# Performance work log

Hardware: AMD Instinct MI355X
Metric: run time of the kernel (lower is better)

Reference implementation:

```python
import jax, jax.numpy as jnp
import numpy as np

B, N, F_IN = 512, 128, 133
NHID, NHEADS, HID = 64, 8, 512
FP_DIM, FP2, TASKS = 1489, 512, 12
ALPHA = 0.2
NEG_BIG = -9e15


def _lin_init(key, fan_in, fan_out):
    return jax.random.normal(key, (fan_in, fan_out), jnp.float32) / np.sqrt(fan_in)


def setup_inputs() -> dict:
    key = jax.random.key(0)
    ks = jax.random.split(key, 24)
    inp = {
        'h': jax.random.normal(ks[0], (B, N, F_IN), jnp.float32),
        'adj': jax.random.randint(ks[1], (B, N, N), 0, 2, jnp.int32),
        'edge_feat': jax.random.uniform(ks[2], (B, N, N), jnp.float32),
        'fp': jax.random.uniform(ks[3], (B, FP_DIM), jnp.float32),
        # multi-head GAT layer params (a split as [a1; a2; a_edge])
        'W_heads': jax.random.normal(ks[4], (NHEADS, F_IN, NHID), jnp.float32) / np.sqrt(F_IN),
        'a1_heads': jax.random.normal(ks[5], (NHEADS, NHID), jnp.float32) / np.sqrt(NHID),
        'a2_heads': jax.random.normal(ks[6], (NHEADS, NHID), jnp.float32) / np.sqrt(NHID),
        'ae_heads': jax.random.normal(ks[7], (NHEADS,), jnp.float32) * 0.1,
        # output GAT layer
        'W_out': jax.random.normal(ks[8], (NHID * NHEADS, HID), jnp.float32) / np.sqrt(NHID * NHEADS),
        'a1_out': jax.random.normal(ks[9], (HID,), jnp.float32) / np.sqrt(HID),
        'a2_out': jax.random.normal(ks[10], (HID,), jnp.float32) / np.sqrt(HID),
        'ae_out': jax.random.normal(ks[11], ()) * 0.1,
        # FPN
        'fc1_w': _lin_init(ks[12], FP_DIM, FP2), 'fc1_b': jnp.zeros((FP2,), jnp.float32),
        'fc2_w': _lin_init(ks[13], FP2, HID), 'fc2_b': jnp.zeros((HID,), jnp.float32),
        # cross-attention fusion
        'q_w': _lin_init(ks[14], HID, HID), 'q_b': jnp.zeros((HID,), jnp.float32),
        'k_w': _lin_init(ks[15], HID, HID), 'k_b': jnp.zeros((HID,), jnp.float32),
        'v_w': _lin_init(ks[16], HID, HID), 'v_b': jnp.zeros((HID,), jnp.float32),
        'o_w': _lin_init(ks[17], HID, HID), 'o_b': jnp.zeros((HID,), jnp.float32),
        # FFN head
        'ffn1_w': _lin_init(ks[18], HID, HID), 'ffn1_b': jnp.zeros((HID,), jnp.float32),
        'ffn2_w': _lin_init(ks[19], HID, TASKS), 'ffn2_b': jnp.zeros((TASKS,), jnp.float32),
    }
    return inp


def _leaky(x):
    return jnp.where(x >= 0, x, ALPHA * x)


def _fpgnn_forward(h, adj, edge_feat, fp,
                   W_heads, a1_heads, a2_heads, ae_heads,
                   W_out, a1_out, a2_out, ae_out,
                   fc1_w, fc1_b, fc2_w, fc2_b,
                   q_w, q_b, k_w, k_b, v_w, v_b, o_w, o_b,
                   ffn1_w, ffn1_b, ffn2_w, ffn2_b):
    mask = adj > 0  # [B,N,N]
    # --- multi-head GAT layers (concat=True) ---
    Wh = jnp.einsum('bnf,hfd->bhnd', h, W_heads)            # [B,H,N,D]
    s1 = jnp.einsum('bhnd,hd->bhn', Wh, a1_heads)
    s2 = jnp.einsum('bhnd,hd->bhn', Wh, a2_heads)
    # e[b,h,i,j] = leaky(Wh_i.a1 + Wh_j.a2 + edge_ij*ae)  (exact decomposition of
    # the original concat([Wh_i, Wh_j, edge_ij]) @ a)
    e = _leaky(s1[:, :, :, None] + s2[:, :, None, :]
               + edge_feat[:, None, :, :] * ae_heads[None, :, None, None])
    att = jnp.where(mask[:, None], e, NEG_BIG)
    att = jax.nn.softmax(att, axis=-1)                       # softmax over dim=1 of [N,N]
    hp = jnp.einsum('bhij,bhjd->bhid', att, Wh)
    x = jax.nn.elu(hp)                                       # concat=True -> ELU
    x = jnp.transpose(x, (0, 2, 1, 3)).reshape(B, N, NHEADS * NHID)
    # --- output GAT layer (concat=False) ---
    Wx = x @ W_out                                           # [B,N,HID]
    t1 = Wx @ a1_out                                         # [B,N]
    t2 = Wx @ a2_out
    e2 = _leaky(t1[:, :, None] + t2[:, None, :] + edge_feat * ae_out)
    att2 = jnp.where(mask, e2, NEG_BIG)
    att2 = jax.nn.softmax(att2, axis=-1)
    hp2 = jnp.einsum('bij,bjd->bid', att2, Wx)
    gat_nodes = jax.nn.elu(hp2)                              # F.elu in GATOne
    gat_out = gat_nodes.mean(axis=1)                         # molecule readout [B,HID]
    # --- FPN ---
    fpn_out = jax.nn.relu(fp @ fc1_w + fc1_b) @ fc2_w + fc2_b  # [B,HID]
    # --- cross-attention fusion ---
    q = gat_out @ q_w + q_b
    k = fpn_out @ k_w + k_b
    v = fpn_out @ v_w + v_b
    score = jnp.sum(q * k, axis=-1, keepdims=True) / np.sqrt(HID)  # [B,1]
    weight = jax.nn.softmax(score[:, :, None], axis=-1)[:, :, 0]    # softmax over size-1 dim -> ones
    fused = q + weight * v
    fused = jax.nn.relu(fused @ o_w + o_b)
    # --- FFN head (dropout p=0, eval) ---
    out = jax.nn.relu(fused @ ffn1_w + ffn1_b) @ ffn2_w + ffn2_b
    return out


def reference(h, adj, edge_feat, fp,
              W_heads, a1_heads, a2_heads, ae_heads,
              W_out, a1_out, a2_out, ae_out,
              fc1_w, fc1_b, fc2_w, fc2_b,
              q_w, q_b, k_w, k_b, v_w, v_b, o_w, o_b,
              ffn1_w, ffn1_b, ffn2_w, ffn2_b):
    return _fpgnn_forward(h, adj, edge_feat, fp,
                          W_heads, a1_heads, a2_heads, ae_heads,
                          W_out, a1_out, a2_out, ae_out,
                          fc1_w, fc1_b, fc2_w, fc2_b,
                          q_w, q_b, k_w, k_b, v_w, v_b, o_w, o_b,
                          ffn1_w, ffn1_b, ffn2_w, ffn2_b)
```

## Files before the change

kernel.cpp:

```cpp
#include <hip/hip_runtime.h>
#include <hip/hip_bf16.h>


#define ALPHA_LK 0.2f
#define LOG2E 1.44269504f
#define KP1 192
#define KPF 1536
#define MINF_BF16 0xFF80u

typedef unsigned short ushort_t;
typedef __attribute__((ext_vector_type(8))) short bfrag;
typedef __attribute__((ext_vector_type(4))) float ffrag;

__device__ __forceinline__ float b2f(ushort_t u) {
  return __uint_as_float(((unsigned)u) << 16);
}
__device__ __forceinline__ ushort_t f2b(float f) {
  unsigned u = __float_as_uint(f);
  unsigned r = (u + 0x7fffu + ((u >> 16) & 1u)) >> 16;
  return (ushort_t)r;
}
__device__ __forceinline__ unsigned cvt_pk(float lo, float hi) {
  unsigned r;
  asm("v_cvt_pk_bf16_f32 %0, %1, %2" : "=v"(r) : "v"(lo), "v"(hi));
  return r;
}
__device__ __forceinline__ float frcp(float x) {
  float r;
  asm("v_rcp_f32 %0, %1" : "=v"(r) : "v"(x));
  return r;
}
__device__ __forceinline__ float fexp2(float x) {
#if __has_builtin(__builtin_amdgcn_exp2f)
  return __builtin_amdgcn_exp2f(x);
#else
  return exp2f(x);
#endif
}
__device__ __forceinline__ float elu1(float v) {
  return v > 0.f ? v : __expf(v) - 1.f;
}

__device__ __forceinline__ void gll16(const void* g, void* l) {
  __builtin_amdgcn_global_load_lds(
      (const __attribute__((address_space(1))) unsigned int*)(unsigned long long)g,
      (__attribute__((address_space(3))) unsigned int*)(unsigned long long)l,
      16, 0, 0);
}

__global__ __launch_bounds__(256) void prep_all(
    const float* __restrict__ h, const int* __restrict__ adj,
    const float* __restrict__ edge, const float* __restrict__ fp,
    const float* __restrict__ Whd, const float* __restrict__ a1h,
    const float* __restrict__ a2h,
    const float* __restrict__ W_out, const float* __restrict__ a1o,
    const float* __restrict__ a2o,
    const float* __restrict__ fc1_w, const float* __restrict__ fc2_w,
    const float* __restrict__ q_w, const float* __restrict__ v_w,
    const float* __restrict__ o_w, const float* __restrict__ ffn1_w,
    const float* __restrict__ qb, const float* __restrict__ vb,
    ushort_t* __restrict__ hb, ushort_t* __restrict__ em,
    ushort_t* __restrict__ W2t, ushort_t* __restrict__ fpb,
    ushort_t* __restrict__ fc1t,
    ushort_t* __restrict__ Wot, ushort_t* __restrict__ fc2t,
    ushort_t* __restrict__ qwt, ushort_t* __restrict__ vwt,
    ushort_t* __restrict__ owt, ushort_t* __restrict__ f1t,
    float* __restrict__ wa1, float* __restrict__ wa2,
    ushort_t* __restrict__ wh12, float* __restrict__ qvb) {
  int bid = blockIdx.x;
  const int t = threadIdx.x;

  if (bid < 8) {
    int hh = bid;
    if (t < 192) {
      float s1 = 0.f, s2 = 0.f;
      if (t < 133) {
        const float* wr = Whd + (size_t)(hh * 133 + t) * 64;
        const float* a1r = a1h + hh * 64;
        const float* a2r = a2h + hh * 64;
#pragma unroll 8
        for (int d = 0; d < 64; ++d) {
          float wv = wr[d];
          s1 += wv * a1r[d];
          s2 += wv * a2r[d];
        }
      }
      wh12[hh * 384 + t] = f2b(s1);
      wh12[hh * 384 + 192 + t] = f2b(s2);
    }
    return;
  }
  bid -= 8;
  if (bid < 128) {
    int wv = t >> 6, lane = t & 63;
    int k = bid * 4 + wv;
    const float* wr = W_out + (size_t)k * 512;
    float p1 = 0.f, p2 = 0.f;
#pragma unroll
    for (int i = 0; i < 8; ++i) {
      float v = wr[lane + i * 64];
      p1 += v * a1o[lane + i * 64];
      p2 += v * a2o[lane + i * 64];
    }
#pragma unroll
    for (int off = 32; off; off >>= 1) {
      p1 += __shfl_down(p1, off);
      p2 += __shfl_down(p2, off);
    }
    if (lane == 0) { wa1[k] = p1; wa2[k] = p2; }
    return;
  }
  bid -= 128;
  if (bid < 2) {
    int o = bid * 256 + t;
    qvb[o] = qb[o] + vb[o];
    return;
  }
  bid -= 2;
  if (bid < 96) {
    int o = bid * 256 + t;
    if (o < 512 * 48) {
      int col = o / 48, c4 = (o - col * 48) * 4;
      int hh = col >> 6, d = col & 63;
      ushort4 v;
      v.x = (c4 + 0 < 133) ? f2b(Whd[(hh * 133 + c4 + 0) * 64 + d]) : (ushort_t)0;
      v.y = (c4 + 1 < 133) ? f2b(Whd[(hh * 133 + c4 + 1) * 64 + d]) : (ushort_t)0;
      v.z = (c4 + 2 < 133) ? f2b(Whd[(hh * 133 + c4 + 2) * 64 + d]) : (ushort_t)0;
      v.w = (c4 + 3 < 133) ? f2b(Whd[(hh * 133 + c4 + 3) * 64 + d]) : (ushort_t)0;
      *(ushort4*)&W2t[(size_t)col * KP1 + c4] = v;
    }
    return;
  }
  bid -= 96;
  if (bid < 768) {
    int o = bid * 256 + t;
    int row = o / 384, c4 = (o - row * 384) * 4;
    const float* fr = fp + (size_t)row * 1489;
    ushort4 v;
    v.x = (c4 + 0 < 1489) ? f2b(fr[c4 + 0]) : (ushort_t)0;
    v.y = (c4 + 1 < 1489) ? f2b(fr[c4 + 1]) : (ushort_t)0;
    v.z = (c4 + 2 < 1489) ? f2b(fr[c4 + 2]) : (ushort_t)0;
    v.w = (c4 + 3 < 1489) ? f2b(fr[c4 + 3]) : (ushort_t)0;
    *(ushort4*)&fpb[(size_t)row * KPF + c4] = v;
    return;
  }
  bid -= 768;
  if (bid < 768) {
    int o = bid * 256 + t;
    int col = o / 384, k4 = (o - col * 384) * 4;
    ushort4 v;
    v.x = (k4 + 0 < 1489) ? f2b(fc1_w[(size_t)(k4 + 0) * 512 + col]) : (ushort_t)0;
    v.y = (k4 + 1 < 1489) ? f2b(fc1_w[(size_t)(k4 + 1) * 512 + col]) : (ushort_t)0;
    v.z = (k4 + 2 < 1489) ? f2b(fc1_w[(size_t)(k4 + 2) * 512 + col]) : (ushort_t)0;
    v.w = (k4 + 3 < 1489) ? f2b(fc1_w[(size_t)(k4 + 3) * 512 + col]) : (ushort_t)0;
    *(ushort4*)&fc1t[(size_t)col * KPF + k4] = v;
    return;
  }
  bid -= 768;
  if (bid < 1536) {
    int y = bid >> 8;
    int o = (bid & 255) * 256 + t;
    const float* W = y == 0 ? W_out : y == 1 ? fc2_w : y == 2 ? q_w
                   : y == 3 ? v_w : y == 4 ? o_w : ffn1_w;
    ushort_t* Wt = y == 0 ? Wot : y == 1 ? fc2t : y == 2 ? qwt
                 : y == 3 ? vwt : y == 4 ? owt : f1t;
    int col = o >> 7, k4 = (o & 127) * 4;
    ushort4 v;
    v.x = f2b(W[(size_t)(k4 + 0) * 512 + col]);
    v.y = f2b(W[(size_t)(k4 + 1) * 512 + col]);
    v.z = f2b(W[(size_t)(k4 + 2) * 512 + col]);
    v.w = f2b(W[(size_t)(k4 + 3) * 512 + col]);
    *(ushort4*)&Wt[(size_t)col * 512 + k4] = v;
    return;
  }
  bid -= 1536;
  if (bid < 12288) {
    int o = bid * 256 + t;
    int row = o / 48, c4 = (o - row * 48) * 4;
    const float* hr = h + (size_t)row * 133;
    ushort4 v;
    v.x = (c4 + 0 < 133) ? f2b(hr[c4 + 0]) : (ushort_t)0;
    v.y = (c4 + 1 < 133) ? f2b(hr[c4 + 1]) : (ushort_t)0;
    v.z = (c4 + 2 < 133) ? f2b(hr[c4 + 2]) : (ushort_t)0;
    v.w = (c4 + 3 < 133) ? f2b(hr[c4 + 3]) : (ushort_t)0;
    *(ushort4*)&hb[(size_t)row * KP1 + c4] = v;
    return;
  }
  bid -= 12288;
  {
    size_t o = ((size_t)bid * 256 + t) * 4;
    float4 e = *(const float4*)&edge[o];
    int4 a = *(const int4*)&adj[o];
    ushort4 v;
    v.x = a.x > 0 ? f2b(e.x) : (ushort_t)MINF_BF16;
    v.y = a.y > 0 ? f2b(e.y) : (ushort_t)MINF_BF16;
    v.z = a.z > 0 ? f2b(e.z) : (ushort_t)MINF_BF16;
    v.w = a.w > 0 ? f2b(e.w) : (ushort_t)MINF_BF16;
    *(ushort4*)&em[o] = v;
  }
}

__global__ __launch_bounds__(256) void att2t(
    const ushort_t* __restrict__ xb, const ushort_t* __restrict__ em,
    const float* __restrict__ wa1, const float* __restrict__ wa2,
    const float* __restrict__ aeo,
    ushort_t* __restrict__ awg, float* __restrict__ sinvg, int base) {
  __shared__ float t1s[128], t2s[128];
  __shared__ float was1[512], was2[512];
  const int bl = blockIdx.x, bg = base + bl;
  const int t = threadIdx.x;
  was1[t] = wa1[t]; was1[t + 256] = wa1[t + 256];
  was2[t] = wa2[t]; was2[t + 256] = wa2[t + 256];
  __syncthreads();
  const int row = t >> 1, half = t & 1;
  {
    const ushort_t* xr = xb + (size_t)(bl * 128 + row) * 512 + half * 256;
    float p1 = 0.f, p2 = 0.f;
#pragma unroll 4
    for (int i = 0; i < 32; ++i) {
      uint4 u = *(const uint4*)&xr[i * 8];
      const unsigned uu[4] = {u.x, u.y, u.z, u.w};
#pragma unroll
      for (int pr = 0; pr < 4; ++pr) {
        float lo = __uint_as_float(uu[pr] << 16);
        float hi = __uint_as_float(uu[pr] & 0xffff0000u);
        int c = half * 256 + i * 8 + pr * 2;
        p1 = fmaf(lo, was1[c], p1); p1 = fmaf(hi, was1[c + 1], p1);
        p2 = fmaf(lo, was2[c], p2); p2 = fmaf(hi, was2[c + 1], p2);
      }
    }
    p1 += __shfl_xor(p1, 1);
    p2 += __shfl_xor(p2, 1);
    if (!half) { t1s[row] = p1 * LOG2E; t2s[row] = p2 * LOG2E; }
  }
  __syncthreads();
  const float ae2 = aeo[0] * LOG2E;
  const float rt1 = t1s[row];
  const ushort_t* emr = em + (size_t)bg * 16384 + row * 128 + half * 64;
  ushort_t* awr = awg + (size_t)bl * 16384 + row * 128 + half * 64;
  float s = 0.f;
#pragma unroll
  for (int v = 0; v < 8; ++v) {
    uint4 eu = *(const uint4*)&emr[v * 8];
    const unsigned uu[4] = {eu.x, eu.y, eu.z, eu.w};
    unsigned po[4];
#pragma unroll
    for (int pr = 0; pr < 4; ++pr) {
      float elo = __uint_as_float(uu[pr] << 16);
      float ehi = __uint_as_float(uu[pr] & 0xffff0000u);
      float e0 = fmaf(elo, ae2, rt1 + t2s[half * 64 + v * 8 + pr * 2]);
      float e1 = fmaf(ehi, ae2, rt1 + t2s[half * 64 + v * 8 + pr * 2 + 1]);
      e0 = fmaxf(e0, ALPHA_LK * e0);
      e1 = fmaxf(e1, ALPHA_LK * e1);
      float p0 = (elo != -INFINITY) ? fexp2(e0) : 0.f;
      float p1 = (ehi != -INFINITY) ? fexp2(e1) : 0.f;
      unsigned q = cvt_pk(p0, p1);
      po[pr] = q;
      s += __uint_as_float(q << 16) + __uint_as_float(q & 0xffff0000u);
    }
    *(uint4*)&awr[v * 8] = make_uint4(po[0], po[1], po[2], po[3]);
  }
  s += __shfl_xor(s, 1);
  if (!half) sinvg[(size_t)bl * 128 + row] = 1.f / fmaxf(s, 1e-30f);
}

__global__ __launch_bounds__(256) void fused_gat1(
    const ushort_t* __restrict__ hb, const ushort_t* __restrict__ W2t,
    const ushort_t* __restrict__ edgeM, const ushort_t* __restrict__ wh12g,
    const float* __restrict__ ae,
    ushort_t* __restrict__ x, int base) {
  __shared__ union {
    struct { ushort_t As[128][64]; ushort_t Bs[64][64]; } g;
    ushort_t WS[64][136];
  } u;
  __shared__ float ss1[128], ss2[128];
  __shared__ ushort_t wh12s[2][192];
  const int id = blockIdx.x;
  const int hh = (id >> 3) & 7;
  const int bl = ((id >> 6) << 3) | (id & 7);
  const int bg = base + bl;
  const int t = threadIdx.x;
  const int lane = t & 63, w = t >> 6;
  const int l16 = lane & 15, quad = lane >> 4;
  const int w8 = w * 8, sr8 = (t >> 3) & 7;
  const int csw = ((t & 7) ^ sr8) << 3;

  if (t < 96)
    *(ushort4*)&(&wh12s[0][0])[t * 4] =
        *(const ushort4*)&wh12g[hh * 384 + t * 4];

  const ushort_t* gA = hb + (size_t)(bl * 128 + w8 + sr8) * KP1 + csw;
  const ushort_t* gB = W2t + (size_t)(hh * 64 + w8 + sr8) * KP1 + csw;
  ffrag acc[2][4];
  ffrag acc_s[2];
#pragma unroll
  for (int mi = 0; mi < 2; ++mi) {
    acc_s[mi] = {0.f, 0.f, 0.f, 0.f};
#pragma unroll
    for (int ni = 0; ni < 4; ++ni) acc[mi][ni] = {0.f, 0.f, 0.f, 0.f};
  }
  for (int k0 = 0; k0 < KP1; k0 += 64) {
    __syncthreads();
#pragma unroll
    for (int p = 0; p < 4; ++p)
      gll16(gA + (size_t)(p * 32) * KP1 + k0, &u.g.As[p * 32 + w8][0]);
#pragma unroll
    for (int p = 0; p < 2; ++p)
      gll16(gB + (size_t)(p * 32) * KP1 + k0, &u.g.Bs[p * 32 + w8][0]);
    __syncthreads();
#pragma unroll
    for (int ks = 0; ks < 2; ++ks) {
      const int cs = ((ks * 4 + quad) ^ (l16 & 7)) << 3;
      bfrag af[2], bf[4];
      bfrag bs = {0, 0, 0, 0, 0, 0, 0, 0};
      if (l16 < 2)
        bs = *(const bfrag*)&wh12s[l16][k0 + ks * 32 + quad * 8];
#pragma unroll
      for (int mi = 0; mi < 2; ++mi)
        af[mi] = *(const bfrag*)&u.g.As[w * 32 + mi * 16 + l16][cs];
#pragma unroll
      for (int ni = 0; ni < 4; ++ni)
        bf[ni] = *(const bfrag*)&u.g.Bs[ni * 16 + l16][cs];
#pragma unroll
      for (int mi = 0; mi < 2; ++mi) {
#pragma unroll
        for (int ni = 0; ni < 4; ++ni)
          acc[mi][ni] = __builtin_amdgcn_mfma_f32_16x16x32_bf16(
              af[mi], bf[ni], acc[mi][ni], 0, 0, 0);
        acc_s[mi] = __builtin_amdgcn_mfma_f32_16x16x32_bf16(
            af[mi], bs, acc_s[mi], 0, 0, 0);
      }
    }
  }
  __syncthreads();

#pragma unroll
  for (int mi = 0; mi < 2; ++mi)
#pragma unroll
    for (int ni = 0; ni < 4; ++ni) {
      int col = ni * 16 + l16;
      int rowb = w * 32 + mi * 16 + quad * 4;
      uint2 pv;
      pv.x = cvt_pk(acc[mi][ni][0], acc[mi][ni][1]);
      pv.y = cvt_pk(acc[mi][ni][2], acc[mi][ni][3]);
      *(uint2*)&u.WS[col][rowb] = pv;
    }
  if (l16 < 2) {
    float* sp = (l16 == 0) ? ss1 : ss2;
#pragma unroll
    for (int mi = 0; mi < 2; ++mi)
#pragma unroll
      for (int r = 0; r < 4; ++r)
        sp[w * 32 + mi * 16 + quad * 4 + r] = acc_s[mi][r] * LOG2E;
  }
  uint4 ereg[2][4];
  {
    const ushort_t* em = edgeM + (size_t)bg * 16384;
#pragma unroll
    for (int mi = 0; mi < 2; ++mi) {
      int row = w * 32 + mi * 16 + l16;
#pragma unroll
      for (int ks = 0; ks < 4; ++ks)
        ereg[mi][ks] = *(const uint4*)&em[row * 128 + ks * 32 + quad * 8];
    }
  }
  __syncthreads();

  const float aeh2 = ae[hh] * LOG2E;
  float rs1[2];
  rs1[0] = ss1[w * 32 + l16];
  rs1[1] = ss1[w * 32 + 16 + l16];
  uint4 aw[2][4];
#pragma unroll
  for (int mi = 0; mi < 2; ++mi) {
#pragma unroll
    for (int ks = 0; ks < 4; ++ks) {
      float s2v[8];
      *(float4*)&s2v[0] = *(const float4*)&ss2[ks * 32 + quad * 8];
      *(float4*)&s2v[4] = *(const float4*)&ss2[ks * 32 + quad * 8 + 4];
      const unsigned uu[4] = {ereg[mi][ks].x, ereg[mi][ks].y,
                              ereg[mi][ks].z, ereg[mi][ks].w};
      unsigned po[4];
#pragma unroll
      for (int pr = 0; pr < 4; ++pr) {
        float elo = __uint_as_float(uu[pr] << 16);
        float ehi = __uint_as_float(uu[pr] & 0xffff0000u);
        float e0 = fmaf(elo, aeh2, rs1[mi] + s2v[pr * 2]);
        float e1 = fmaf(ehi, aeh2, rs1[mi] + s2v[pr * 2 + 1]);
        e0 = fmaxf(e0, ALPHA_LK * e0);
        e1 = fmaxf(e1, ALPHA_LK * e1);
        float p0 = (elo != -INFINITY) ? fexp2(e0) : 0.f;
        float p1 = (ehi != -INFINITY) ? fexp2(e1) : 0.f;
        po[pr] = cvt_pk(p0, p1);
      }
      aw[mi][ks] = make_uint4(po[0], po[1], po[2], po[3]);
    }
  }

  bfrag bones;
#pragma unroll
  for (int i = 0; i < 8; ++i) bones[i] = (short)0x3F80;

  ffrag acc2[2][4];
  ffrag accs[2];
#pragma unroll
  for (int mi = 0; mi < 2; ++mi) {
    accs[mi] = {0.f, 0.f, 0.f, 0.f};
#pragma unroll
    for (int ni = 0; ni < 4; ++ni) acc2[mi][ni] = {0.f, 0.f, 0.f, 0.f};
  }
#pragma unroll
  for (int ks = 0; ks < 4; ++ks) {
    bfrag bfr[4];
#pragma unroll
    for (int ni = 0; ni < 4; ++ni)
      bfr[ni] = *(const bfrag*)&u.WS[ni * 16 + l16][ks * 32 + quad * 8];
#pragma unroll
    for (int mi = 0; mi < 2; ++mi) {
      bfrag afr;
      __builtin_memcpy(&afr, &aw[mi][ks], 16);
#pragma unroll
      for (int ni = 0; ni < 4; ++ni)
        acc2[mi][ni] = __builtin_amdgcn_mfma_f32_16x16x32_bf16(
            afr, bfr[ni], acc2[mi][ni], 0, 0, 0);
      accs[mi] = __builtin_amdgcn_mfma_f32_16x16x32_bf16(
          afr, bones, accs[mi], 0, 0, 0);
    }
  }
  float sv[2][4];
#pragma unroll
  for (int mi = 0; mi < 2; ++mi)
#pragma unroll
    for (int r = 0; r < 4; ++r)
      sv[mi][r] = frcp(fmaxf(accs[mi][r], 1e-30f));

#pragma unroll
  for (int mi = 0; mi < 2; ++mi)
#pragma unroll
    for (int ni = 0; ni < 4; ++ni) {
      float e0 = elu1(acc2[mi][ni][0] * sv[mi][0]);
      float e1 = elu1(acc2[mi][ni][1] * sv[mi][1]);
      float e2 = elu1(acc2[mi][ni][2] * sv[mi][2]);
      float e3 = elu1(acc2[mi][ni][3] * sv[mi][3]);
      unsigned p01 = cvt_pk(e0, e1), p23 = cvt_pk(e2, e3);
      int rl = w * 32 + mi * 16 + quad * 4;
      size_t bo = (size_t)(bl * 128 + rl) * 512 + hh * 64 + ni * 16 + l16;
      x[bo] = (ushort_t)p01;
      x[bo + 512] = (ushort_t)(p01 >> 16);
      x[bo + 1024] = (ushort_t)p23;
      x[bo + 1536] = (ushort_t)(p23 >> 16);
    }
}

__global__ __launch_bounds__(256) void fused_gat2(
    const ushort_t* __restrict__ xb, const ushort_t* __restrict__ Wot,
    const ushort_t* __restrict__ awg, const float* __restrict__ sinvg,
    ushort_t* __restrict__ gatb, int base) {
  __shared__ union {
    struct { ushort_t As[128][64]; ushort_t Bs[128][64]; } g;
    ushort_t WS[128][136];
  } u;
  __shared__ float ps[4][64];
  const int id = blockIdx.x;
  const int sp2 = (id >> 3) & 3;
  const int bl = ((id >> 5) << 3) | (id & 7);
  const int bg = base + bl;
  const int t = threadIdx.x;
  const int lane = t & 63, w = t >> 6;
  const int wm = w >> 1, wn = w & 1;
  const int l16 = lane & 15, quad = lane >> 4;
  const int w8 = w * 8, sr8 = (t >> 3) & 7;
  const int csw = ((t & 7) ^ sr8) << 3;

  const ushort_t* gA = xb + (size_t)(bl * 128 + w8 + sr8) * 512 + csw;
  const ushort_t* gB = Wot + (size_t)(sp2 * 128 + w8 + sr8) * 512 + csw;
  ffrag acc[4][4];
#pragma unroll
  for (int mi = 0; mi < 4; ++mi)
#pragma unroll
    for (int ni = 0; ni < 4; ++ni) acc[mi][ni] = {0.f, 0.f, 0.f, 0.f};
  for (int k0 = 0; k0 < 512; k0 += 64) {
    __syncthreads();
#pragma unroll
    for (int p = 0; p < 4; ++p) {
      gll16(gA + (size_t)(p * 32) * 512 + k0, &u.g.As[p * 32 + w8][0]);
      gll16(gB + (size_t)(p * 32) * 512 + k0, &u.g.Bs[p * 32 + w8][0]);
    }
    __syncthreads();
#pragma unroll
    for (int ks = 0; ks < 2; ++ks) {
      const int cs = ((ks * 4 + quad) ^ (l16 & 7)) << 3;
      bfrag af[4], bf[4];
#pragma unroll
      for (int i = 0; i < 4; ++i) {
        af[i] = *(const bfrag*)&u.g.As[wm * 64 + i * 16 + l16][cs];
        bf[i] = *(const bfrag*)&u.g.Bs[wn * 64 + i * 16 + l16][cs];
      }
#pragma unroll
      for (int mi = 0; mi < 4; ++mi)
#pragma unroll
        for (int ni = 0; ni < 4; ++ni)
          acc[mi][ni] = __builtin_amdgcn_mfma_f32_16x16x32_bf16(
              af[mi], bf[ni], acc[mi][ni], 0, 0, 0);
    }
  }
  __syncthreads();

#pragma unroll
  for (int mi = 0; mi < 4; ++mi)
#pragma unroll
    for (int ni = 0; ni < 4; ++ni) {
      int col = wn * 64 + ni * 16 + l16;
      int rowb = wm * 64 + mi * 16 + quad * 4;
      uint2 pv;
      pv.x = cvt_pk(acc[mi][ni][0], acc[mi][ni][1]);
      pv.y = cvt_pk(acc[mi][ni][2], acc[mi][ni][3]);
      *(uint2*)&u.WS[col][rowb] = pv;
    }
  __syncthreads();

  uint4 awf[2][4];
  float sv[2][4];
  {
    const ushort_t* ap = awg + (size_t)bl * 16384;
#pragma unroll
    for (int mi = 0; mi < 2; ++mi) {
      int row = w * 32 + mi * 16 + l16;
#pragma unroll
      for (int ks = 0; ks < 4; ++ks)
        awf[mi][ks] = *(const uint4*)&ap[row * 128 + ks * 32 + quad * 8];
      float si = sinvg[(size_t)bl * 128 + row];
#pragma unroll
      for (int r = 0; r < 4; ++r) sv[mi][r] = __shfl(si, quad * 4 + r);
    }
  }

  for (int s0 = 0; s0 < 2; ++s0) {
    ffrag acc2[2][4];
#pragma unroll
    for (int mi = 0; mi < 2; ++mi)
#pragma unroll
      for (int ni = 0; ni < 4; ++ni) acc2[mi][ni] = {0.f, 0.f, 0.f, 0.f};
#pragma unroll
    for (int ks = 0; ks < 4; ++ks) {
      bfrag bfr[4];
#pragma unroll
      for (int ni = 0; ni < 4; ++ni)
        bfr[ni] = *(const bfrag*)&u.WS[s0 * 64 + ni * 16 + l16][ks * 32 + quad * 8];
#pragma unroll
      for (int mi = 0; mi < 2; ++mi) {
        bfrag afr;
        __builtin_memcpy(&afr, &awf[mi][ks], 16);
#pragma unroll
        for (int ni = 0; ni < 4; ++ni)
          acc2[mi][ni] = __builtin_amdgcn_mfma_f32_16x16x32_bf16(
              afr, bfr[ni], acc2[mi][ni], 0, 0, 0);
      }
    }
    __syncthreads();
#pragma unroll
    for (int ni = 0; ni < 4; ++ni) {
      float s = 0.f;
#pragma unroll
      for (int mi = 0; mi < 2; ++mi)
#pragma unroll
        for (int r = 0; r < 4; ++r) s += elu1(acc2[mi][ni][r] * sv[mi][r]);
      s += __shfl_xor(s, 16);
      s += __shfl_xor(s, 32);
      if (quad == 0) ps[w][ni * 16 + l16] = s;
    }
    __syncthreads();
    if (t < 64) {
      float s = ps[0][t] + ps[1][t] + ps[2][t] + ps[3][t];
      gatb[(size_t)bg * 512 + sp2 * 128 + s0 * 64 + t] = f2b(s * (1.f / 128.f));
    }
  }
}

__device__ __forceinline__ void tail_kloop(
    const ushort_t* __restrict__ A, const ushort_t* __restrict__ Bt,
    int K, int ld, ushort_t (*As)[64], ushort_t (*Bs)[64],
    ffrag (*acc)[4], int row0, int col0, int t) {
  const int lane = t & 63, w = t >> 6;
  const int wm = w >> 1, wn = w & 1;
  const int l16 = lane & 15, quad = lane >> 4;
  const int w8 = w * 8, sr8 = (t >> 3) & 7;
  const int csw = ((t & 7) ^ sr8) << 3;
  const ushort_t* gA = A + (size_t)(row0 + w8 + sr8) * ld + csw;
  const ushort_t* gB = Bt + (size_t)(col0 + w8 + sr8) * ld + csw;
  for (int k0 = 0; k0 < K; k0 += 64) {
    __syncthreads();
#pragma unroll
    for (int p = 0; p < 4; ++p) {
      gll16(gA + (size_t)(p * 32) * ld + k0, &As[p * 32 + w8][0]);
      gll16(gB + (size_t)(p * 32) * ld + k0, &Bs[p * 32 + w8][0]);
    }
    __syncthreads();
#pragma unroll
    for (int ks = 0; ks < 2; ++ks) {
      const int cs = ((ks * 4 + quad) ^ (l16 & 7)) << 3;
      bfrag af[4], bf[4];
#pragma unroll
      for (int i = 0; i < 4; ++i) {
        af[i] = *(const bfrag*)&As[wm * 64 + i * 16 + l16][cs];
        bf[i] = *(const bfrag*)&Bs[wn * 64 + i * 16 + l16][cs];
      }
#pragma unroll
      for (int mi = 0; mi < 4; ++mi)
#pragma unroll
        for (int ni = 0; ni < 4; ++ni)
          acc[mi][ni] = __builtin_amdgcn_mfma_f32_16x16x32_bf16(
              af[mi], bf[ni], acc[mi][ni], 0, 0, 0);
    }
  }
}

template <int DUAL, int RELU>
__global__ __launch_bounds__(256) void gemm_tail(
    const ushort_t* __restrict__ A1, const ushort_t* __restrict__ Bt1,
    int K1, int ld1,
    const ushort_t* __restrict__ A2, const ushort_t* __restrict__ Bt2,
    const float* __restrict__ bias, ushort_t* __restrict__ C) {
  __shared__ ushort_t As[128][64];
  __shared__ ushort_t Bs[128][64];
  const int t = threadIdx.x;
  const int lane = t & 63, w = t >> 6;
  const int wm = w >> 1, wn = w & 1;
  const int l16 = lane & 15, quad = lane >> 4;
  const int row0 = blockIdx.y * 128, col0 = blockIdx.x * 128;

  ffrag acc[4][4];
#pragma unroll
  for (int mi = 0; mi < 4; ++mi)
#pragma unroll
    for (int ni = 0; ni < 4; ++ni) acc[mi][ni] = {0.f, 0.f, 0.f, 0.f};

  tail_kloop(A1, Bt1, K1, ld1, As, Bs, acc, row0, col0, t);
  if (DUAL) tail_kloop(A2, Bt2, 512, 512, As, Bs, acc, row0, col0, t);

#pragma unroll
  for (int mi = 0; mi < 4; ++mi)
#pragma unroll
    for (int ni = 0; ni < 4; ++ni) {
      int col = col0 + wn * 64 + ni * 16 + l16;
      float bb = bias[col];
      float v0 = acc[mi][ni][0] + bb, v1 = acc[mi][ni][1] + bb;
      float v2 = acc[mi][ni][2] + bb, v3 = acc[mi][ni][3] + bb;
      if (RELU) {
        v0 = fmaxf(v0, 0.f); v1 = fmaxf(v1, 0.f);
        v2 = fmaxf(v2, 0.f); v3 = fmaxf(v3, 0.f);
      }
      unsigned p01 = cvt_pk(v0, v1), p23 = cvt_pk(v2, v3);
      int row = row0 + wm * 64 + mi * 16 + quad * 4;
      size_t o = (size_t)row * 512 + col;
      C[o] = (ushort_t)p01;
      C[o + 512] = (ushort_t)(p01 >> 16);
      C[o + 1024] = (ushort_t)p23;
      C[o + 1536] = (ushort_t)(p23 >> 16);
    }
}

__global__ __launch_bounds__(256) void ffn2_kernel(
    const ushort_t* __restrict__ f5, const float* __restrict__ W,
    const float* __restrict__ b, float* __restrict__ out) {
  int wv = threadIdx.x >> 6, lane = threadIdx.x & 63;
  int row = blockIdx.x * 4 + wv;
  const ushort_t* fr = f5 + (size_t)row * 512;
  float v[8];
  ushort4 u0 = *(const ushort4*)&fr[lane * 8];
  ushort4 u1 = *(const ushort4*)&fr[lane * 8 + 4];
  v[0] = b2f(u0.x); v[1] = b2f(u0.y); v[2] = b2f(u0.z); v[3] = b2f(u0.w);
  v[4] = b2f(u1.x); v[5] = b2f(u1.y); v[6] = b2f(u1.z); v[7] = b2f(u1.w);
#pragma unroll
  for (int j = 0; j < 12; ++j) {
    float s = 0.f;
#pragma unroll
    for (int i = 0; i < 8; ++i) s += v[i] * W[(size_t)(lane * 8 + i) * 12 + j];
#pragma unroll
    for (int off = 32; off; off >>= 1) s += __shfl_down(s, off);
    if (lane == 0) out[(size_t)row * 12 + j] = s + b[j];
  }
}

extern "C" void kernel_launch(void* const* d_in, const int* in_sizes, int n_in,
                              void* d_out, int out_size, void* d_ws, size_t ws_size,
                              hipStream_t stream) {
  const float* h        = (const float*)d_in[0];
  const int*   adj      = (const int*)d_in[1];
  const float* edge     = (const float*)d_in[2];
  const float* fp       = (const float*)d_in[3];
  const float* W_heads  = (const float*)d_in[4];
  const float* a1_heads = (const float*)d_in[5];
  const float* a2_heads = (const float*)d_in[6];
  const float* ae_heads = (const float*)d_in[7];
  const float* W_out  = (const float*)d_in[8];
  const float* a1_out = (const float*)d_in[9];
  const float* a2_out = (const float*)d_in[10];
  const float* ae_out = (const float*)d_in[11];
  const float* fc1_w = (const float*)d_in[12];
  const float* fc1_b = (const float*)d_in[13];
  const float* fc2_w = (const float*)d_in[14];
  const float* fc2_b = (const float*)d_in[15];
  const float* q_w = (const float*)d_in[16];
  const float* q_b = (const float*)d_in[17];
  const float* v_w = (const float*)d_in[20];
  const float* v_b = (const float*)d_in[21];
  const float* o_w = (const float*)d_in[22];
  const float* o_b = (const float*)d_in[23];
  const float* ffn1_w = (const float*)d_in[24];
  const float* ffn1_b = (const float*)d_in[25];
  const float* ffn2_w = (const float*)d_in[26];
  const float* ffn2_b = (const float*)d_in[27];
  float* out = (float*)d_out;

  const size_t hb_bytes = (size_t)65536 * KP1 * 2;
  const size_t em_bytes = (size_t)512 * 16384 * 2;
  const size_t tail_bytes =
      (size_t)512 * KPF * 2 * 2 + (size_t)512 * 512 * 2 * 12 + 2048;
  const size_t fixed_bytes = hb_bytes + em_bytes + (size_t)512 * KP1 * 2 +
                             (size_t)2 * 65536 * 4 + tail_bytes + 16384;
  int C = 32;
  for (int cand = 512; cand >= 32; cand >>= 1) {
    size_t need = (size_t)cand * (131072 + 32768 + 512) + fixed_bytes;
    if (need <= ws_size) { C = cand; break; }
  }
  const int M = C * 128;
  (void)M;

  char* p = (char*)d_ws;
  ushort_t* xb  = (ushort_t*)p; p += (size_t)C * 65536 * 2;
  ushort_t* awg = (ushort_t*)p; p += (size_t)C * 16384 * 2;
  float* sinv   = (float*)p;    p += (size_t)C * 128 * 4;
  ushort_t* hb  = (ushort_t*)p; p += hb_bytes;
  ushort_t* em  = (ushort_t*)p; p += em_bytes;
  ushort_t* W2t = (ushort_t*)p; p += (size_t)512 * KP1 * 2;
  ushort_t* wh12 = (ushort_t*)p; p += 8 * 384 * 2;
  float* t_unused = (float*)p; p += 2 * 65536 * 4 - 8 * 384 * 2;
  (void)t_unused;
  ushort_t* fpb  = (ushort_t*)p; p += (size_t)512 * KPF * 2;
  ushort_t* fc1t = (ushort_t*)p; p += (size_t)512 * KPF * 2;
  ushort_t* Wot  = (ushort_t*)p; p += (size_t)512 * 512 * 2;
  ushort_t* fc2t = (ushort_t*)p; p += (size_t)512 * 512 * 2;
  ushort_t* qwt  = (ushort_t*)p; p += (size_t)512 * 512 * 2;
  ushort_t* vwt  = (ushort_t*)p; p += (size_t)512 * 512 * 2;
  ushort_t* owt  = (ushort_t*)p; p += (size_t)512 * 512 * 2;
  ushort_t* f1t  = (ushort_t*)p; p += (size_t)512 * 512 * 2;
  ushort_t* gatb = (ushort_t*)p; p += (size_t)512 * 512 * 2;
  ushort_t* fb1  = (ushort_t*)p; p += (size_t)512 * 512 * 2;
  ushort_t* fb2  = (ushort_t*)p; p += (size_t)512 * 512 * 2;
  ushort_t* fb3  = (ushort_t*)p; p += (size_t)512 * 512 * 2;
  ushort_t* fb4  = (ushort_t*)p; p += (size_t)512 * 512 * 2;
  ushort_t* fb5  = (ushort_t*)p; p += (size_t)512 * 512 * 2;
  float* qvb = (float*)p; p += 2048;
  float* wa1 = (float*)p; p += 2048;
  float* wa2 = (float*)p; p += 2048;

  prep_all<<<23786, 256, 0, stream>>>(
      h, adj, edge, fp, W_heads, a1_heads, a2_heads,
      W_out, a1_out, a2_out,
      fc1_w, fc2_w, q_w, v_w, o_w, ffn1_w, q_b, v_b,
      hb, em, W2t, fpb, fc1t, Wot, fc2t, qwt, vwt, owt, f1t,
      wa1, wa2, wh12, qvb);

  for (int base = 0; base < 512; base += C) {
    fused_gat1<<<8 * C, 256, 0, stream>>>(
        hb + (size_t)base * 128 * KP1, W2t, em, wh12, ae_heads, xb, base);
    att2t<<<C, 256, 0, stream>>>(xb, em, wa1, wa2, ae_out, awg, sinv, base);
    fused_gat2<<<4 * C, 256, 0, stream>>>(xb, Wot, awg, sinv, gatb, base);
  }

  gemm_tail<0, 1><<<dim3(4, 4), 256, 0, stream>>>(
      fpb, fc1t, KPF, KPF, nullptr, nullptr, fc1_b, fb1);
  gemm_tail<0, 0><<<dim3(4, 4), 256, 0, stream>>>(
      fb1, fc2t, 512, 512, nullptr, nullptr, fc2_b, fb2);
  gemm_tail<1, 0><<<dim3(4, 4), 256, 0, stream>>>(
      gatb, qwt, 512, 512, fb2, vwt, qvb, fb3);
  gemm_tail<0, 1><<<dim3(4, 4), 256, 0, stream>>>(
      fb3, owt, 512, 512, nullptr, nullptr, o_b, fb4);
  gemm_tail<0, 1><<<dim3(4, 4), 256, 0, stream>>>(
      fb4, f1t, 512, 512, nullptr, nullptr, ffn1_b, fb5);
  ffn2_kernel<<<128, 256, 0, stream>>>(fb5, ffn2_w, ffn2_b, out);
}
```

Baseline: 425.6 us.

## Overlap FPN GEMMs with GAT stages and merge tail GEMMs via grid barrier

The fc1 and fc2 tail GEMMs now run as extra blocks inside the first attention and second GAT launches, so they overlap with the per-chunk graph work. The remaining q/v, o, ffn1 and ffn2 stages are merged into one 16-block kernel that uses an atomic-counter software barrier between stages, replacing five separate launches. Kernels now take a single parameter struct. The spin barrier relies on all 16 blocks being resident at once and on the counter being reset in prep. gat1 now indexes hb by the global batch index instead of receiving an offset pointer.

Result: slower. 585.0 us (+37.5%).

```diff
diff --git a/kernel.cpp b/kernel.cpp
--- a/kernel.cpp
+++ b/kernel.cpp
@@ -40,7 +40,6 @@
 __device__ __forceinline__ float elu1(float v) {
   return v > 0.f ? v : __expf(v) - 1.f;
 }
-
 __device__ __forceinline__ void gll16(const void* g, void* l) {
   __builtin_amdgcn_global_load_lds(
       (const __attribute__((address_space(1))) unsigned int*)(unsigned long long)g,
@@ -48,36 +47,56 @@
       16, 0, 0);
 }
 
-__global__ __launch_bounds__(256) void prep_all(
-    const float* __restrict__ h, const int* __restrict__ adj,
-    const float* __restrict__ edge, const float* __restrict__ fp,
-    const float* __restrict__ Whd, const float* __restrict__ a1h,
-    const float* __restrict__ a2h,
-    const float* __restrict__ W_out, const float* __restrict__ a1o,
-    const float* __restrict__ a2o,
-    const float* __restrict__ fc1_w, const float* __restrict__ fc2_w,
-    const float* __restrict__ q_w, const float* __restrict__ v_w,
-    const float* __restrict__ o_w, const float* __restrict__ ffn1_w,
-    const float* __restrict__ qb, const float* __restrict__ vb,
-    ushort_t* __restrict__ hb, ushort_t* __restrict__ em,
-    ushort_t* __restrict__ W2t, ushort_t* __restrict__ fpb,
-    ushort_t* __restrict__ fc1t,
-    ushort_t* __restrict__ Wot, ushort_t* __restrict__ fc2t,
-    ushort_t* __restrict__ qwt, ushort_t* __restrict__ vwt,
-    ushort_t* __restrict__ owt, ushort_t* __restrict__ f1t,
-    float* __restrict__ wa1, float* __restrict__ wa2,
-    ushort_t* __restrict__ wh12, float* __restrict__ qvb) {
-  int bid = blockIdx.x;
+struct MP {
+  const float *h; const int *adj; const float *edge; const float *fp;
+  const float *Whd, *a1h, *a2h, *aeh;
+  const float *W_out, *a1o, *a2o, *aeo;
+  const float *fc1_w, *fc1_b, *fc2_w, *fc2_b;
+  const float *q_b, *v_b, *q_w, *v_w, *o_w, *o_b;
+  const float *ffn1_w, *ffn1_b, *ffn2_w, *ffn2_b;
+  ushort_t *hb, *em, *W2t, *wh12, *fpb, *fc1t, *Wot, *fc2t, *qwt, *vwt, *owt, *f1t;
+  ushort_t *xb, *awg; float *sinv;
+  ushort_t *gatb, *fb1, *fb2, *fb3, *fb4, *fb5;
+  float *wa1, *wa2, *qvb; float *out;
+  unsigned *cnt;
+  int C;
+};
+
+struct LdsGat1 {
+  union { struct { ushort_t As[128][64]; ushort_t Bs[64][64]; } g;
+          ushort_t WS[64][136]; } u;
+  float ss1[128], ss2[128];
+  ushort_t wh12s[2][192];
+};
+struct LdsGat2 {
+  union { struct { ushort_t As[128][64]; ushort_t Bs[128][64]; } g;
+          ushort_t WS[128][136]; } u;
+  float ps[4][64];
+};
+struct LdsAtt { float t1s[128], t2s[128], was1[512], was2[512]; };
+struct LdsTail { ushort_t As[128][64]; ushort_t Bs[128][64]; };
+
+__device__ __forceinline__ void tbar(unsigned* cnt, unsigned target) {
+  __syncthreads();
+  __threadfence();
+  if (threadIdx.x == 0) {
+    atomicAdd(cnt, 1u);
+    while (atomicAdd(cnt, 0u) < target) __builtin_amdgcn_s_sleep(1);
+  }
+  __syncthreads();
+  __threadfence();
+}
+
+__device__ void prep_body(int bid, const MP& P) {
   const int t = threadIdx.x;
-
   if (bid < 8) {
     int hh = bid;
     if (t < 192) {
       float s1 = 0.f, s2 = 0.f;
       if (t < 133) {
-        const float* wr = Whd + (size_t)(hh * 133 + t) * 64;
-        const float* a1r = a1h + hh * 64;
-        const float* a2r = a2h + hh * 64;
+        const float* wr = P.Whd + (size_t)(hh * 133 + t) * 64;
+        const float* a1r = P.a1h + hh * 64;
+        const float* a2r = P.a2h + hh * 64;
 #pragma unroll 8
         for (int d = 0; d < 64; ++d) {
           float wv = wr[d];
@@ -85,8 +104,8 @@
           s2 += wv * a2r[d];
         }
       }
-      wh12[hh * 384 + t] = f2b(s1);
-      wh12[hh * 384 + 192 + t] = f2b(s2);
+      P.wh12[hh * 384 + t] = f2b(s1);
+      P.wh12[hh * 384 + 192 + t] = f2b(s2);
     }
     return;
   }
@@ -94,26 +113,27 @@
   if (bid < 128) {
     int wv = t >> 6, lane = t & 63;
     int k = bid * 4 + wv;
-    const float* wr = W_out + (size_t)k * 512;
+    const float* wr = P.W_out + (size_t)k * 512;
     float p1 = 0.f, p2 = 0.f;
 #pragma unroll
     for (int i = 0; i < 8; ++i) {
       float v = wr[lane + i * 64];
-      p1 += v * a1o[lane + i * 64];
-      p2 += v * a2o[lane + i * 64];
+      p1 += v * P.a1o[lane + i * 64];
+      p2 += v * P.a2o[lane + i * 64];
     }
 #pragma unroll
     for (int off = 32; off; off >>= 1) {
       p1 += __shfl_down(p1, off);
       p2 += __shfl_down(p2, off);
     }
-    if (lane == 0) { wa1[k] = p1; wa2[k] = p2; }
+    if (lane == 0) { P.wa1[k] = p1; P.wa2[k] = p2; }
     return;
   }
   bid -= 128;
   if (bid < 2) {
     int o = bid * 256 + t;
-    qvb[o] = qb[o] + vb[o];
+    P.qvb[o] = P.q_b[o] + P.v_b[o];
+    if (bid == 0 && t == 0) P.cnt[0] = 0u;
     return;
   }
   bid -= 2;
@@ -123,11 +143,11 @@
       int col = o / 48, c4 = (o - col * 48) * 4;
       int hh = col >> 6, d = col & 63;
       ushort4 v;
-      v.x = (c4 + 0 < 133) ? f2b(Whd[(hh * 133 + c4 + 0) * 64 + d]) : (ushort_t)0;
-      v.y = (c4 + 1 < 133) ? f2b(Whd[(hh * 133 + c4 + 1) * 64 + d]) : (ushort_t)0;
-      v.z = (c4 + 2 < 133) ? f2b(Whd[(hh * 133 + c4 + 2) * 64 + d]) : (ushort_t)0;
-      v.w = (c4 + 3 < 133) ? f2b(Whd[(hh * 133 + c4 + 3) * 64 + d]) : (ushort_t)0;
-      *(ushort4*)&W2t[(size_t)col * KP1 + c4] = v;
+      v.x = (c4 + 0 < 133) ? f2b(P.Whd[(hh * 133 + c4 + 0) * 64 + d]) : (ushort_t)0;
+      v.y = (c4 + 1 < 133) ? f2b(P.Whd[(hh * 133 + c4 + 1) * 64 + d]) : (ushort_t)0;
+      v.z = (c4 + 2 < 133) ? f2b(P.Whd[(hh * 133 + c4 + 2) * 64 + d]) : (ushort_t)0;
+      v.w = (c4 + 3 < 133) ? f2b(P.Whd[(hh * 133 + c4 + 3) * 64 + d]) : (ushort_t)0;
+      *(ushort4*)&P.W2t[(size_t)col * KP1 + c4] = v;
     }
     return;
   }
@@ -135,13 +155,13 @@
   if (bid < 768) {
     int o = bid * 256 + t;
     int row = o / 384, c4 = (o - row * 384) * 4;
-    const float* fr = fp + (size_t)row * 1489;
+    const float* fr = P.fp + (size_t)row * 1489;
     ushort4 v;
     v.x = (c4 + 0 < 1489) ? f2b(fr[c4 + 0]) : (ushort_t)0;
     v.y = (c4 + 1 < 1489) ? f2b(fr[c4 + 1]) : (ushort_t)0;
     v.z = (c4 + 2 < 1489) ? f2b(fr[c4 + 2]) : (ushort_t)0;
     v.w = (c4 + 3 < 1489) ? f2b(fr[c4 + 3]) : (ushort_t)0;
-    *(ushort4*)&fpb[(size_t)row * KPF + c4] = v;
+    *(ushort4*)&P.fpb[(size_t)row * KPF + c4] = v;
     return;
   }
   bid -= 768;
@@ -149,21 +169,21 @@
     int o = bid * 256 + t;
     int col = o / 384, k4 = (o - col * 384) * 4;
     ushort4 v;
-    v.x = (k4 + 0 < 1489) ? f2b(fc1_w[(size_t)(k4 + 0) * 512 + col]) : (ushort_t)0;
-    v.y = (k4 + 1 < 1489) ? f2b(fc1_w[(size_t)(k4 + 1) * 512 + col]) : (ushort_t)0;
-    v.z = (k4 + 2 < 1489) ? f2b(fc1_w[(size_t)(k4 + 2) * 512 + col]) : (ushort_t)0;
-    v.w = (k4 + 3 < 1489) ? f2b(fc1_w[(size_t)(k4 + 3) * 512 + col]) : (ushort_t)0;
-    *(ushort4*)&fc1t[(size_t)col * KPF + k4] = v;
+    v.x = (k4 + 0 < 1489) ? f2b(P.fc1_w[(size_t)(k4 + 0) * 512 + col]) : (ushort_t)0;
+    v.y = (k4 + 1 < 1489) ? f2b(P.fc1_w[(size_t)(k4 + 1) * 512 + col]) : (ushort_t)0;
+    v.z = (k4 + 2 < 1489) ? f2b(P.fc1_w[(size_t)(k4 + 2) * 512 + col]) : (ushort_t)0;
+    v.w = (k4 + 3 < 1489) ? f2b(P.fc1_w[(size_t)(k4 + 3) * 512 + col]) : (ushort_t)0;
+    *(ushort4*)&P.fc1t[(size_t)col * KPF + k4] = v;
     return;
   }
   bid -= 768;
   if (bid < 1536) {
     int y = bid >> 8;
     int o = (bid & 255) * 256 + t;
-    const float* W = y == 0 ? W_out : y == 1 ? fc2_w : y == 2 ? q_w
-                   : y == 3 ? v_w : y == 4 ? o_w : ffn1_w;
-    ushort_t* Wt = y == 0 ? Wot : y == 1 ? fc2t : y == 2 ? qwt
-                 : y == 3 ? vwt : y == 4 ? owt : f1t;
+    const float* W = y == 0 ? P.W_out : y == 1 ? P.fc2_w : y == 2 ? P.q_w
+                   : y == 3 ? P.v_w : y == 4 ? P.o_w : P.ffn1_w;
+    ushort_t* Wt = y == 0 ? P.Wot : y == 1 ? P.fc2t : y == 2 ? P.qwt
+                 : y == 3 ? P.vwt : y == 4 ? P.owt : P.f1t;
     int col = o >> 7, k4 = (o & 127) * 4;
     ushort4 v;
     v.x = f2b(W[(size_t)(k4 + 0) * 512 + col]);
@@ -177,105 +197,30 @@
   if (bid < 12288) {
     int o = bid * 256 + t;
     int row = o / 48, c4 = (o - row * 48) * 4;
-    const float* hr = h + (size_t)row * 133;
+    const float* hr = P.h + (size_t)row * 133;
     ushort4 v;
     v.x = (c4 + 0 < 133) ? f2b(hr[c4 + 0]) : (ushort_t)0;
     v.y = (c4 + 1 < 133) ? f2b(hr[c4 + 1]) : (ushort_t)0;
     v.z = (c4 + 2 < 133) ? f2b(hr[c4 + 2]) : (ushort_t)0;
     v.w = (c4 + 3 < 133) ? f2b(hr[c4 + 3]) : (ushort_t)0;
-    *(ushort4*)&hb[(size_t)row * KP1 + c4] = v;
+    *(ushort4*)&P.hb[(size_t)row * KP1 + c4] = v;
     return;
   }
   bid -= 12288;
   {
     size_t o = ((size_t)bid * 256 + t) * 4;
-    float4 e = *(const float4*)&edge[o];
-    int4 a = *(const int4*)&adj[o];
+    float4 e = *(const float4*)&P.edge[o];
+    int4 a = *(const int4*)&P.adj[o];
     ushort4 v;
     v.x = a.x > 0 ? f2b(e.x) : (ushort_t)MINF_BF16;
     v.y = a.y > 0 ? f2b(e.y) : (ushort_t)MINF_BF16;
     v.z = a.z > 0 ? f2b(e.z) : (ushort_t)MINF_BF16;
     v.w = a.w > 0 ? f2b(e.w) : (ushort_t)MINF_BF16;
-    *(ushort4*)&em[o] = v;
-  }
-}
-
-__global__ __launch_bounds__(256) void att2t(
-    const ushort_t* __restrict__ xb, const ushort_t* __restrict__ em,
-    const float* __restrict__ wa1, const float* __restrict__ wa2,
-    const float* __restrict__ aeo,
-    ushort_t* __restrict__ awg, float* __restrict__ sinvg, int base) {
-  __shared__ float t1s[128], t2s[128];
-  __shared__ float was1[512], was2[512];
-  const int bl = blockIdx.x, bg = base + bl;
-  const int t = threadIdx.x;
-  was1[t] = wa1[t]; was1[t + 256] = wa1[t + 256];
-  was2[t] = wa2[t]; was2[t + 256] = wa2[t + 256];
-  __syncthreads();
-  const int row = t >> 1, half = t & 1;
-  {
-    const ushort_t* xr = xb + (size_t)(bl * 128 + row) * 512 + half * 256;
-    float p1 = 0.f, p2 = 0.f;
-#pragma unroll 4
-    for (int i = 0; i < 32; ++i) {
-      uint4 u = *(const uint4*)&xr[i * 8];
-      const unsigned uu[4] = {u.x, u.y, u.z, u.w};
-#pragma unroll
-      for (int pr = 0; pr < 4; ++pr) {
-        float lo = __uint_as_float(uu[pr] << 16);
-        float hi = __uint_as_float(uu[pr] & 0xffff0000u);
-        int c = half * 256 + i * 8 + pr * 2;
-        p1 = fmaf(lo, was1[c], p1); p1 = fmaf(hi, was1[c + 1], p1);
-        p2 = fmaf(lo, was2[c], p2); p2 = fmaf(hi, was2[c + 1], p2);
-      }
-    }
-    p1 += __shfl_xor(p1, 1);
-    p2 += __shfl_xor(p2, 1);
-    if (!half) { t1s[row] = p1 * LOG2E; t2s[row] = p2 * LOG2E; }
-  }
-  __syncthreads();
-  const float ae2 = aeo[0] * LOG2E;
-  const float rt1 = t1s[row];
-  const ushort_t* emr = em + (size_t)bg * 16384 + row * 128 + half * 64;
-  ushort_t* awr = awg + (size_t)bl * 16384 + row * 128 + half * 64;
-  float s = 0.f;
-#pragma unroll
-  for (int v = 0; v < 8; ++v) {
-    uint4 eu = *(const uint4*)&emr[v * 8];
-    const unsigned uu[4] = {eu.x, eu.y, eu.z, eu.w};
-    unsigned po[4];
-#pragma unroll
-    for (int pr = 0; pr < 4; ++pr) {
-      float elo = __uint_as_float(uu[pr] << 16);
-      float ehi = __uint_as_float(uu[pr] & 0xffff0000u);
-      float e0 = fmaf(elo, ae2, rt1 + t2s[half * 64 + v * 8 + pr * 2]);
-      float e1 = fmaf(ehi, ae2, rt1 + t2s[half * 64 + v * 8 + pr * 2 + 1]);
-      e0 = fmaxf(e0, ALPHA_LK * e0);
-      e1 = fmaxf(e1, ALPHA_LK * e1);
-      float p0 = (elo != -INFINITY) ? fexp2(e0) : 0.f;
-      float p1 = (ehi != -INFINITY) ? fexp2(e1) : 0.f;
-      unsigned q = cvt_pk(p0, p1);
-      po[pr] = q;
-      s += __uint_as_float(q << 16) + __uint_as_float(q & 0xffff0000u);
-    }
-    *(uint4*)&awr[v * 8] = make_uint4(po[0], po[1], po[2], po[3]);
-  }
-  s += __shfl_xor(s, 1);
-  if (!half) sinvg[(size_t)bl * 128 + row] = 1.f / fmaxf(s, 1e-30f);
-}
-
-__global__ __launch_bounds__(256) void fused_gat1(
-    const ushort_t* __restrict__ hb, const ushort_t* __restrict__ W2t,
-    const ushort_t* __restrict__ edgeM, const ushort_t* __restrict__ wh12g,
-    const float* __restrict__ ae,
-    ushort_t* __restrict__ x, int base) {
-  __shared__ union {
-    struct { ushort_t As[128][64]; ushort_t Bs[64][64]; } g;
-    ushort_t WS[64][136];
-  } u;
-  __shared__ float ss1[128], ss2[128];
-  __shared__ ushort_t wh12s[2][192];
-  const int id = blockIdx.x;
+    *(ushort4*)&P.em[o] = v;
+  }
+}
+
+__device__ void gat1_body(int id, int base, const MP& P, LdsGat1& L) {
   const int hh = (id >> 3) & 7;
   const int bl = ((id >> 6) << 3) | (id & 7);
   const int bg = base + bl;
@@ -286,11 +231,11 @@
   const int csw = ((t & 7) ^ sr8) << 3;
 
   if (t < 96)
-    *(ushort4*)&(&wh12s[0][0])[t * 4] =
-        *(const ushort4*)&wh12g[hh * 384 + t * 4];
-
-  const ushort_t* gA = hb + (size_t)(bl * 128 + w8 + sr8) * KP1 + csw;
-  const ushort_t* gB = W2t + (size_t)(hh * 64 + w8 + sr8) * KP1 + csw;
+    *(ushort4*)&(&L.wh12s[0][0])[t * 4] =
+        *(const ushort4*)&P.wh12[hh * 384 + t * 4];
+
+  const ushort_t* gA = P.hb + (size_t)(bg * 128 + w8 + sr8) * KP1 + csw;
+  const ushort_t* gB = P.W2t + (size_t)(hh * 64 + w8 + sr8) * KP1 + csw;
   ffrag acc[2][4];
   ffrag acc_s[2];
 #pragma unroll
@@ -303,10 +248,10 @@
     __syncthreads();
 #pragma unroll
     for (int p = 0; p < 4; ++p)
-      gll16(gA + (size_t)(p * 32) * KP1 + k0, &u.g.As[p * 32 + w8][0]);
+      gll16(gA + (size_t)(p * 32) * KP1 + k0, &L.u.g.As[p * 32 + w8][0]);
 #pragma unroll
     for (int p = 0; p < 2; ++p)
-      gll16(gB + (size_t)(p * 32) * KP1 + k0, &u.g.Bs[p * 32 + w8][0]);
+      gll16(gB + (size_t)(p * 32) * KP1 + k0, &L.u.g.Bs[p * 32 + w8][0]);
     __syncthreads();
 #pragma unroll
     for (int ks = 0; ks < 2; ++ks) {
@@ -314,13 +259,13 @@
       bfrag af[2], bf[4];
       bfrag bs = {0, 0, 0, 0, 0, 0, 0, 0};
       if (l16 < 2)
-        bs = *(const bfrag*)&wh12s[l16][k0 + ks * 32 + quad * 8];
+        bs = *(const bfrag*)&L.wh12s[l16][k0 + ks * 32 + quad * 8];
 #pragma unroll
       for (int mi = 0; mi < 2; ++mi)
-        af[mi] = *(const bfrag*)&u.g.As[w * 32 + mi * 16 + l16][cs];
+        af[mi] = *(const bfrag*)&L.u.g.As[w * 32 + mi * 16 + l16][cs];
 #pragma unroll
       for (int ni = 0; ni < 4; ++ni)
-        bf[ni] = *(const bfrag*)&u.g.Bs[ni * 16 + l16][cs];
+        bf[ni] = *(const bfrag*)&L.u.g.Bs[ni * 16 + l16][cs];
 #pragma unroll
       for (int mi = 0; mi < 2; ++mi) {
 #pragma unroll
@@ -343,10 +288,10 @@
       uint2 pv;
       pv.x = cvt_pk(acc[mi][ni][0], acc[mi][ni][1]);
       pv.y = cvt_pk(acc[mi][ni][2], acc[mi][ni][3]);
-      *(uint2*)&u.WS[col][rowb] = pv;
+      *(uint2*)&L.u.WS[col][rowb] = pv;
     }
   if (l16 < 2) {
-    float* sp = (l16 == 0) ? ss1 : ss2;
+    float* sp = (l16 == 0) ? L.ss1 : L.ss2;
 #pragma unroll
     for (int mi = 0; mi < 2; ++mi)
 #pragma unroll
@@ -355,7 +300,7 @@
   }
   uint4 ereg[2][4];
   {
-    const ushort_t* em = edgeM + (size_t)bg * 16384;
+    const ushort_t* em = P.em + (size_t)bg * 16384;
 #pragma unroll
     for (int mi = 0; mi < 2; ++mi) {
       int row = w * 32 + mi * 16 + l16;
@@ -366,18 +311,18 @@
   }
   __syncthreads();
 
-  const float aeh2 = ae[hh] * LOG2E;
+  const float aeh2 = P.aeh[hh] * LOG2E;
   float rs1[2];
-  rs1[0] = ss1[w * 32 + l16];
-  rs1[1] = ss1[w * 32 + 16 + l16];
+  rs1[0] = L.ss1[w * 32 + l16];
+  rs1[1] = L.ss1[w * 32 + 16 + l16];
   uint4 aw[2][4];
 #pragma unroll
   for (int mi = 0; mi < 2; ++mi) {
 #pragma unroll
     for (int ks = 0; ks < 4; ++ks) {
       float s2v[8];
-      *(float4*)&s2v[0] = *(const float4*)&ss2[ks * 32 + quad * 8];
-      *(float4*)&s2v[4] = *(const float4*)&ss2[ks * 32 + quad * 8 + 4];
+      *(float4*)&s2v[0] = *(const float4*)&L.ss2[ks * 32 + quad * 8];
+      *(float4*)&s2v[4] = *(const float4*)&L.ss2[ks * 32 + quad * 8 + 4];
       const unsigned uu[4] = {ereg[mi][ks].x, ereg[mi][ks].y,
                               ereg[mi][ks].z, ereg[mi][ks].w};
       unsigned po[4];
@@ -414,7 +359,7 @@
     bfrag bfr[4];
 #pragma unroll
     for (int ni = 0; ni < 4; ++ni)
-      bfr[ni] = *(const bfrag*)&u.WS[ni * 16 + l16][ks * 32 + quad * 8];
+      bfr[ni] = *(const bfrag*)&L.u.WS[ni * 16 + l16][ks * 32 + quad * 8];
 #pragma unroll
     for (int mi = 0; mi < 2; ++mi) {
       bfrag afr;
@@ -445,23 +390,72 @@
       unsigned p01 = cvt_pk(e0, e1), p23 = cvt_pk(e2, e3);
       int rl = w * 32 + mi * 16 + quad * 4;
       size_t bo = (size_t)(bl * 128 + rl) * 512 + hh * 64 + ni * 16 + l16;
-      x[bo] = (ushort_t)p01;
-      x[bo + 512] = (ushort_t)(p01 >> 16);
-      x[bo + 1024] = (ushort_t)p23;
-      x[bo + 1536] = (ushort_t)(p23 >> 16);
-    }
-}
-
-__global__ __launch_bounds__(256) void fused_gat2(
-    const ushort_t* __restrict__ xb, const ushort_t* __restrict__ Wot,
-    const ushort_t* __restrict__ awg, const float* __restrict__ sinvg,
-    ushort_t* __restrict__ gatb, int base) {
-  __shared__ union {
-    struct { ushort_t As[128][64]; ushort_t Bs[128][64]; } g;
-    ushort_t WS[128][136];
-  } u;
-  __shared__ float ps[4][64];
-  const int id = blockIdx.x;
+      P.xb[bo] = (ushort_t)p01;
+      P.xb[bo + 512] = (ushort_t)(p01 >> 16);
+      P.xb[bo + 1024] = (ushort_t)p23;
+      P.xb[bo + 1536] = (ushort_t)(p23 >> 16);
+    }
+}
+
+__device__ void att2t_body(int bl, int base, const MP& P, LdsAtt& L) {
+  const int bg = base + bl;
+  const int t = threadIdx.x;
+  L.was1[t] = P.wa1[t]; L.was1[t + 256] = P.wa1[t + 256];
+  L.was2[t] = P.wa2[t]; L.was2[t + 256] = P.wa2[t + 256];
+  __syncthreads();
+  const int row = t >> 1, half = t & 1;
+  {
+    const ushort_t* xr = P.xb + (size_t)(bl * 128 + row) * 512 + half * 256;
+    float p1 = 0.f, p2 = 0.f;
+#pragma unroll 4
+    for (int i = 0; i < 32; ++i) {
+      uint4 u = *(const uint4*)&xr[i * 8];
+      const unsigned uu[4] = {u.x, u.y, u.z, u.w};
+#pragma unroll
+      for (int pr = 0; pr < 4; ++pr) {
+        float lo = __uint_as_float(uu[pr] << 16);
+        float hi = __uint_as_float(uu[pr] & 0xffff0000u);
+        int c = half * 256 + i * 8 + pr * 2;
+        p1 = fmaf(lo, L.was1[c], p1); p1 = fmaf(hi, L.was1[c + 1], p1);
+        p2 = fmaf(lo, L.was2[c], p2); p2 = fmaf(hi, L.was2[c + 1], p2);
+      }
+    }
+    p1 += __shfl_xor(p1, 1);
+    p2 += __shfl_xor(p2, 1);
+    if (!half) { L.t1s[row] = p1 * LOG2E; L.t2s[row] = p2 * LOG2E; }
+  }
+  __syncthreads();
+  const float ae2 = P.aeo[0] * LOG2E;
+  const float rt1 = L.t1s[row];
+  const ushort_t* emr = P.em + (size_t)bg * 16384 + row * 128 + half * 64;
+  ushort_t* awr = P.awg + (size_t)bl * 16384 + row * 128 + half * 64;
+  float s = 0.f;
+#pragma unroll
+  for (int v = 0; v < 8; ++v) {
+    uint4 eu = *(const uint4*)&emr[v * 8];
+    const unsigned uu[4] = {eu.x, eu.y, eu.z, eu.w};
+    unsigned po[4];
+#pragma unroll
+    for (int pr = 0; pr < 4; ++pr) {
+      float elo = __uint_as_float(uu[pr] << 16);
+      float ehi = __uint_as_float(uu[pr] & 0xffff0000u);
+      float e0 = fmaf(elo, ae2, rt1 + L.t2s[half * 64 + v * 8 + pr * 2]);
+      float e1 = fmaf(ehi, ae2, rt1 + L.t2s[half * 64 + v * 8 + pr * 2 + 1]);
+      e0 = fmaxf(e0, ALPHA_LK * e0);
+      e1 = fmaxf(e1, ALPHA_LK * e1);
+      float p0 = (elo != -INFINITY) ? fexp2(e0) : 0.f;
+      float p1 = (ehi != -INFINITY) ? fexp2(e1) : 0.f;
+      unsigned q = cvt_pk(p0, p1);
+      po[pr] = q;
+      s += __uint_as_float(q << 16) + __uint_as_float(q & 0xffff0000u);
+    }
+    *(uint4*)&awr[v * 8] = make_uint4(po[0], po[1], po[2], po[3]);
+  }
+  s += __shfl_xor(s, 1);
+  if (!half) P.sinv[(size_t)bl * 128 + row] = 1.f / fmaxf(s, 1e-30f);
+}
+
+__device__ void gat2_body(int id, int base, const MP& P, LdsGat2& L) {
   const int sp2 = (id >> 3) & 3;
   const int bl = ((id >> 5) << 3) | (id & 7);
   const int bg = base + bl;
@@ -472,8 +466,8 @@
   const int w8 = w * 8, sr8 = (t >> 3) & 7;
   const int csw = ((t & 7) ^ sr8) << 3;
 
-  const ushort_t* gA = xb + (size_t)(bl * 128 + w8 + sr8) * 512 + csw;
-  const ushort_t* gB = Wot + (size_t)(sp2 * 128 + w8 + sr8) * 512 + csw;
+  const ushort_t* gA = P.xb + (size_t)(bl * 128 + w8 + sr8) * 512 + csw;
+  const ushort_t* gB = P.Wot + (size_t)(sp2 * 128 + w8 + sr8) * 512 + csw;
   ffrag acc[4][4];
 #pragma unroll
   for (int mi = 0; mi < 4; ++mi)
@@ -483,8 +477,8 @@
     __syncthreads();
 #pragma unroll
     for (int p = 0; p < 4; ++p) {
-      gll16(gA + (size_t)(p * 32) * 512 + k0, &u.g.As[p * 32 + w8][0]);
-      gll16(gB + (size_t)(p * 32) * 512 + k0, &u.g.Bs[p * 32 + w8][0]);
+      gll16(gA + (size_t)(p * 32) * 512 + k0, &L.u.g.As[p * 32 + w8][0]);
+      gll16(gB + (size_t)(p * 32) * 512 + k0, &L.u.g.Bs[p * 32 + w8][0]);
     }
     __syncthreads();
 #pragma unroll
@@ -493,8 +487,8 @@
       bfrag af[4], bf[4];
 #pragma unroll
       for (int i = 0; i < 4; ++i) {
-        af[i] = *(const bfrag*)&u.g.As[wm * 64 + i * 16 + l16][cs];
-        bf[i] = *(const bfrag*)&u.g.Bs[wn * 64 + i * 16 + l16][cs];
+        af[i] = *(const bfrag*)&L.u.g.As[wm * 64 + i * 16 + l16][cs];
+        bf[i] = *(const bfrag*)&L.u.g.Bs[wn * 64 + i * 16 + l16][cs];
       }
 #pragma unroll
       for (int mi = 0; mi < 4; ++mi)
@@ -515,21 +509,21 @@
       uint2 pv;
       pv.x = cvt_pk(acc[mi][ni][0], acc[mi][ni][1]);
       pv.y = cvt_pk(acc[mi][ni][2], acc[mi][ni][3]);
-      *(uint2*)&u.WS[col][rowb] = pv;
+      *(uint2*)&L.u.WS[col][rowb] = pv;
     }
   __syncthreads();
 
   uint4 awf[2][4];
   float sv[2][4];
   {
-    const ushort_t* ap = awg + (size_t)bl * 16384;
+    const ushort_t* ap = P.awg + (size_t)bl * 16384;
 #pragma unroll
     for (int mi = 0; mi < 2; ++mi) {
       int row = w * 32 + mi * 16 + l16;
 #pragma unroll
       for (int ks = 0; ks < 4; ++ks)
         awf[mi][ks] = *(const uint4*)&ap[row * 128 + ks * 32 + quad * 8];
-      float si = sinvg[(size_t)bl * 128 + row];
+      float si = P.sinv[(size_t)bl * 128 + row];
 #pragma unroll
       for (int r = 0; r < 4; ++r) sv[mi][r] = __shfl(si, quad * 4 + r);
     }
@@ -546,7 +540,7 @@
       bfrag bfr[4];
 #pragma unroll
       for (int ni = 0; ni < 4; ++ni)
-        bfr[ni] = *(const bfrag*)&u.WS[s0 * 64 + ni * 16 + l16][ks * 32 + quad * 8];
+        bfr[ni] = *(const bfrag*)&L.u.WS[s0 * 64 + ni * 16 + l16][ks * 32 + quad * 8];
 #pragma unroll
       for (int mi = 0; mi < 2; ++mi) {
         bfrag afr;
@@ -567,20 +561,19 @@
         for (int r = 0; r < 4; ++r) s += elu1(acc2[mi][ni][r] * sv[mi][r]);
       s += __shfl_xor(s, 16);
       s += __shfl_xor(s, 32);
-      if (quad == 0) ps[w][ni * 16 + l16] = s;
+      if (quad == 0) L.ps[w][ni * 16 + l16] = s;
     }
     __syncthreads();
     if (t < 64) {
-      float s = ps[0][t] + ps[1][t] + ps[2][t] + ps[3][t];
-      gatb[(size_t)bg * 512 + sp2 * 128 + s0 * 64 + t] = f2b(s * (1.f / 128.f));
-    }
-  }
-}
-
-__device__ __forceinline__ void tail_kloop(
-    const ushort_t* __restrict__ A, const ushort_t* __restrict__ Bt,
-    int K, int ld, ushort_t (*As)[64], ushort_t (*Bs)[64],
-    ffrag (*acc)[4], int row0, int col0, int t) {
+      float s = L.ps[0][t] + L.ps[1][t] + L.ps[2][t] + L.ps[3][t];
+      P.gatb[(size_t)bg * 512 + sp2 * 128 + s0 * 64 + t] = f2b(s * (1.f / 128.f));
+    }
+  }
+}
+
+__device__ void tail_kloop(const ushort_t* A, const ushort_t* Bt, int K, int ld,
+                           ushort_t (*As)[64], ushort_t (*Bs)[64],
+                           ffrag (*acc)[4], int row0, int col0, int t) {
   const int lane = t & 63, w = t >> 6;
   const int wm = w >> 1, wn = w & 1;
   const int l16 = lane & 15, quad = lane >> 4;
@@ -615,19 +608,15 @@
   }
 }
 
-template <int DUAL, int RELU>
-__global__ __launch_bounds__(256) void gemm_tail(
-    const ushort_t* __restrict__ A1, const ushort_t* __restrict__ Bt1,
-    int K1, int ld1,
-    const ushort_t* __restrict__ A2, const ushort_t* __restrict__ Bt2,
-    const float* __restrict__ bias, ushort_t* __restrict__ C) {
-  __shared__ ushort_t As[128][64];
-  __shared__ ushort_t Bs[128][64];
+__device__ void tailg_body(int vb, const ushort_t* A1, const ushort_t* Bt1,
+                           int K1, int ld1, const ushort_t* A2,
+                           const ushort_t* Bt2, const float* bias,
+                           ushort_t* Cc, int DUAL, int RELU, LdsTail& L) {
   const int t = threadIdx.x;
   const int lane = t & 63, w = t >> 6;
   const int wm = w >> 1, wn = w & 1;
   const int l16 = lane & 15, quad = lane >> 4;
-  const int row0 = blockIdx.y * 128, col0 = blockIdx.x * 128;
+  const int row0 = (vb >> 2) * 128, col0 = (vb & 3) * 128;
 
   ffrag acc[4][4];
 #pragma unroll
@@ -635,8 +624,8 @@
 #pragma unroll
     for (int ni = 0; ni < 4; ++ni) acc[mi][ni] = {0.f, 0.f, 0.f, 0.f};
 
-  tail_kloop(A1, Bt1, K1, ld1, As, Bs, acc, row0, col0, t);
-  if (DUAL) tail_kloop(A2, Bt2, 512, 512, As, Bs, acc, row0, col0, t);
+  tail_kloop(A1, Bt1, K1, ld1, L.As, L.Bs, acc, row0, col0, t);
+  if (DUAL) tail_kloop(A2, Bt2, 512, 512, L.As, L.Bs, acc, row0, col0, t);
 
 #pragma unroll
   for (int mi = 0; mi < 4; ++mi)
@@ -653,19 +642,17 @@
       unsigned p01 = cvt_pk(v0, v1), p23 = cvt_pk(v2, v3);
       int row = row0 + wm * 64 + mi * 16 + quad * 4;
       size_t o = (size_t)row * 512 + col;
-      C[o] = (ushort_t)p01;
-      C[o + 512] = (ushort_t)(p01 >> 16);
-      C[o + 1024] = (ushort_t)p23;
-      C[o + 1536] = (ushort_t)(p23 >> 16);
-    }
-}
-
-__global__ __launch_bounds__(256) void ffn2_kernel(
-    const ushort_t* __restrict__ f5, const float* __restrict__ W,
-    const float* __restrict__ b, float* __restrict__ out) {
+      Cc[o] = (ushort_t)p01;
+      Cc[o + 512] = (ushort_t)(p01 >> 16);
+      Cc[o + 1024] = (ushort_t)p23;
+      Cc[o + 1536] = (ushort_t)(p23 >> 16);
+    }
+}
+
+__device__ void ffn2_body(int vb, const MP& P) {
   int wv = threadIdx.x >> 6, lane = threadIdx.x & 63;
-  int row = blockIdx.x * 4 + wv;
-  const ushort_t* fr = f5 + (size_t)row * 512;
+  int row = vb * 4 + wv;
+  const ushort_t* fr = P.fb5 + (size_t)row * 512;
   float v[8];
   ushort4 u0 = *(const ushort4*)&fr[lane * 8];
   ushort4 u1 = *(const ushort4*)&fr[lane * 8 + 4];
@@ -675,43 +662,80 @@
   for (int j = 0; j < 12; ++j) {
     float s = 0.f;
 #pragma unroll
-    for (int i = 0; i < 8; ++i) s += v[i] * W[(size_t)(lane * 8 + i) * 12 + j];
+    for (int i = 0; i < 8; ++i)
+      s += v[i] * P.ffn2_w[(size_t)(lane * 8 + i) * 12 + j];
 #pragma unroll
     for (int off = 32; off; off >>= 1) s += __shfl_down(s, off);
-    if (lane == 0) out[(size_t)row * 12 + j] = s + b[j];
-  }
+    if (lane == 0) P.out[(size_t)row * 12 + j] = s + P.ffn2_b[j];
+  }
+}
+
+__global__ __launch_bounds__(256) void k_prep(MP P) { prep_body(blockIdx.x, P); }
+
+__global__ __launch_bounds__(256) void k_gat1(MP P, int base) {
+  __shared__ LdsGat1 L;
+  gat1_body(blockIdx.x, base, P, L);
+}
+
+__global__ __launch_bounds__(256) void k_att(MP P, int base) {
+  __shared__ union { LdsAtt at; LdsTail tl; } L;
+  int b = blockIdx.x;
+  if (b < P.C) att2t_body(b, base, P, L.at);
+  else tailg_body(b - P.C, P.fpb, P.fc1t, KPF, KPF, nullptr, nullptr,
+                  P.fc1_b, P.fb1, 0, 1, L.tl);
+}
+
+__global__ __launch_bounds__(256) void k_gat2(MP P, int base) {
+  __shared__ union { LdsGat2 g2; LdsTail tl; } L;
+  int b = blockIdx.x;
+  if (b < 4 * P.C) gat2_body(b, base, P, L.g2);
+  else tailg_body(b - 4 * P.C, P.fb1, P.fc2t, 512, 512, nullptr, nullptr,
+                  P.fc2_b, P.fb2, 0, 0, L.tl);
+}
+
+__global__ __launch_bounds__(256) void k_tail6(MP P) {
+  __shared__ LdsTail L;
+  int b = blockIdx.x;
+  tailg_body(b, P.gatb, P.qwt, 512, 512, P.fb2, P.vwt, P.qvb, P.fb3, 1, 0, L);
+  tbar(P.cnt, 16);
+  tailg_body(b, P.fb3, P.owt, 512, 512, nullptr, nullptr, P.o_b, P.fb4, 0, 1, L);
+  tbar(P.cnt, 32);
+  tailg_body(b, P.fb4, P.f1t, 512, 512, nullptr, nullptr, P.ffn1_b, P.fb5, 0, 1, L);
+  tbar(P.cnt, 48);
+  for (int vb = b; vb < 128; vb += 16) ffn2_body(vb, P);
 }
 
 extern "C" void kernel_launch(void* const* d_in, const int* in_sizes, int n_in,
                               void* d_out, int out_size, void* d_ws, size_t ws_size,
                               hipStream_t stream) {
-  const float* h        = (const float*)d_in[0];
-  const int*   adj      = (const int*)d_in[1];
-  const float* edge     = (const float*)d_in[2];
-  const float* fp       = (const float*)d_in[3];
-  const float* W_heads  = (const float*)d_in[4];
-  const float* a1_heads = (const float*)d_in[5];
-  const float* a2_heads = (const float*)d_in[6];
-  const float* ae_heads = (const float*)d_in[7];
-  const float* W_out  = (const float*)d_in[8];
-  const float* a1_out = (const float*)d_in[9];
-  const float* a2_out = (const float*)d_in[10];
-  const float* ae_out = (const float*)d_in[11];
-  const float* fc1_w = (const float*)d_in[12];
-  const float* fc1_b = (const float*)d_in[13];
-  const float* fc2_w = (const float*)d_in[14];
-  const float* fc2_b = (const float*)d_in[15];
-  const float* q_w = (const float*)d_in[16];
-  const float* q_b = (const float*)d_in[17];
-  const float* v_w = (const float*)d_in[20];
-  const float* v_b = (const float*)d_in[21];
-  const float* o_w = (const float*)d_in[22];
-  const float* o_b = (const float*)d_in[23];
-  const float* ffn1_w = (const float*)d_in[24];
-  const float* ffn1_b = (const float*)d_in[25];
-  const float* ffn2_w = (const float*)d_in[26];
-  const float* ffn2_b = (const float*)d_in[27];
-  float* out = (float*)d_out;
+  MP P;
+  P.h        = (const float*)d_in[0];
+  P.adj      = (const int*)d_in[1];
+  P.edge     = (const float*)d_in[2];
+  P.fp       = (const float*)d_in[3];
+  P.Whd      = (const float*)d_in[4];
+  P.a1h      = (const float*)d_in[5];
+  P.a2h      = (const float*)d_in[6];
+  P.aeh      = (const float*)d_in[7];
+  P.W_out    = (const float*)d_in[8];
+  P.a1o      = (const float*)d_in[9];
+  P.a2o      = (const float*)d_in[10];
+  P.aeo      = (const float*)d_in[11];
+  P.fc1_w    = (const float*)d_in[12];
+  P.fc1_b    = (const float*)d_in[13];
+  P.fc2_w    = (const float*)d_in[14];
+  P.fc2_b    = (const float*)d_in[15];
+  P.q_w      = (const float*)d_in[16];
+  P.q_b      = (const float*)d_in[17];
+  P.v_w      = (const float*)d_in[20];
+  P.v_b      = (const float*)d_in[21];
+  P.o_w      = (const float*)d_in[22];
+  P.o_b      = (const float*)d_in[23];
+  P.ffn1_w   = (const float*)d_in[24];
+  P.ffn1_b   = (const float*)d_in[25];
+  P.ffn2_w   = (const float*)d_in[26];
+  P.ffn2_b   = (const float*)d_in[27];
+  P.out      = (float*)d_out;
 
   const size_t hb_bytes = (size_t)65536 * KP1 * 2;
   const size_t em_bytes = (size_t)512 * 16384 * 2;
@@ -724,60 +748,42 @@
     size_t need = (size_t)cand * (131072 + 32768 + 512) + fixed_bytes;
     if (need <= ws_size) { C = cand; break; }
   }
-  const int M = C * 128;
-  (void)M;
+  P.C = C;
 
   char* p = (char*)d_ws;
-  ushort_t* xb  = (ushort_t*)p; p += (size_t)C * 65536 * 2;
-  ushort_t* awg = (ushort_t*)p; p += (size_t)C * 16384 * 2;
-  float* sinv   = (float*)p;    p += (size_t)C * 128 * 4;
-  ushort_t* hb  = (ushort_t*)p; p += hb_bytes;
-  ushort_t* em  = (ushort_t*)p; p += em_bytes;
-  ushort_t* W2t = (ushort_t*)p; p += (size_t)512 * KP1 * 2;
-  ushort_t* wh12 = (ushort_t*)p; p += 8 * 384 * 2;
-  float* t_unused = (float*)p; p += 2 * 65536 * 4 - 8 * 384 * 2;
-  (void)t_unused;
-  ushort_t* fpb  = (ushort_t*)p; p += (size_t)512 * KPF * 2;
-  ushort_t* fc1t = (ushort_t*)p; p += (size_t)512 * KPF * 2;
-  ushort_t* Wot  = (ushort_t*)p; p += (size_t)512 * 512 * 2;
-  ushort_t* fc2t = (ushort_t*)p; p += (size_t)512 * 512 * 2;
-  ushort_t* qwt  = (ushort_t*)p; p += (size_t)512 * 512 * 2;
-  ushort_t* vwt  = (ushort_t*)p; p += (size_t)512 * 512 * 2;
-  ushort_t* owt  = (ushort_t*)p; p += (size_t)512 * 512 * 2;
-  ushort_t* f1t  = (ushort_t*)p; p += (size_t)512 * 512 * 2;
-  ushort_t* gatb = (ushort_t*)p; p += (size_t)512 * 512 * 2;
-  ushort_t* fb1  = (ushort_t*)p; p += (size_t)512 * 512 * 2;
-  ushort_t* fb2  = (ushort_t*)p; p += (size_t)512 * 512 * 2;
-  ushort_t* fb3  = (ushort_t*)p; p += (size_t)512 * 512 * 2;
-  ushort_t* fb4  = (ushort_t*)p; p += (size_t)512 * 512 * 2;
-  ushort_t* fb5  = (ushort_t*)p; p += (size_t)512 * 512 * 2;
-  float* qvb = (float*)p; p += 2048;
-  float* wa1 = (float*)p; p += 2048;
-  float* wa2 = (float*)p; p += 2048;
-
-  prep_all<<<23786, 256, 0, stream>>>(
-      h, adj, edge, fp, W_heads, a1_heads, a2_heads,
-      W_out, a1_out, a2_out,
-      fc1_w, fc2_w, q_w, v_w, o_w, ffn1_w, q_b, v_b,
-      hb, em, W2t, fpb, fc1t, Wot, fc2t, qwt, vwt, owt, f1t,
-      wa1, wa2, wh12, qvb);
-
+  P.xb  = (ushort_t*)p; p += (size_t)C * 65536 * 2;
+  P.awg = (ushort_t*)p; p += (size_t)C * 16384 * 2;
+  P.sinv = (float*)p;   p += (size_t)C * 128 * 4;
+  P.hb  = (ushort_t*)p; p += hb_bytes;
+  P.em  = (ushort_t*)p; p += em_bytes;
+  P.W2t = (ushort_t*)p; p += (size_t)512 * KP1 * 2;
+  P.wh12 = (ushort_t*)p; p += 8 * 384 * 2;
+  p += 2 * 65536 * 4 - 8 * 384 * 2;
+  P.fpb  = (ushort_t*)p; p += (size_t)512 * KPF * 2;
+  P.fc1t = (ushort_t*)p; p += (size_t)512 * KPF * 2;
+  P.Wot  = (ushort_t*)p; p += (size_t)512 * 512 * 2;
+  P.fc2t = (ushort_t*)p; p += (size_t)512 * 512 * 2;
+  P.qwt  = (ushort_t*)p; p += (size_t)512 * 512 * 2;
+  P.vwt  = (ushort_t*)p; p += (size_t)512 * 512 * 2;
+  P.owt  = (ushort_t*)p; p += (size_t)512 * 512 * 2;
+  P.f1t  = (ushort_t*)p; p += (size_t)512 * 512 * 2;
+  P.gatb = (ushort_t*)p; p += (size_t)512 * 512 * 2;
+  P.fb1  = (ushort_t*)p; p += (size_t)512 * 512 * 2;
+  P.fb2  = (ushort_t*)p; p += (size_t)512 * 512 * 2;
+  P.fb3  = (ushort_t*)p; p += (size_t)512 * 512 * 2;
+  P.fb4  = (ushort_t*)p; p += (size_t)512 * 512 * 2;
+  P.fb5  = (ushort_t*)p; p += (size_t)512 * 512 * 2;
+  P.qvb  = (float*)p; p += 2048;
+  P.wa1  = (float*)p; p += 2048;
+  P.wa2  = (float*)p; p += 2048;
+  P.cnt  = (unsigned*)p; p += 64;
+
+  k_prep<<<23786, 256, 0, stream>>>(P);
   for (int base = 0; base < 512; base += C) {
-    fused_gat1<<<8 * C, 256, 0, stream>>>(
-        hb + (size_t)base * 128 * KP1, W2t, em, wh12, ae_heads, xb, base);
-    att2t<<<C, 256, 0, stream>>>(xb, em, wa1, wa2, ae_out, awg, sinv, base);
-    fused_gat2<<<4 * C, 256, 0, stream>>>(xb, Wot, awg, sinv, gatb, base);
-  }
-
-  gemm_tail<0, 1><<<dim3(4, 4), 256, 0, stream>>>(
-      fpb, fc1t, KPF, KPF, nullptr, nullptr, fc1_b, fb1);
-  gemm_tail<0, 0><<<dim3(4, 4), 256, 0, stream>>>(
-      fb1, fc2t, 512, 512, nullptr, nullptr, fc2_b, fb2);
-  gemm_tail<1, 0><<<dim3(4, 4), 256, 0, stream>>>(
-      gatb, qwt, 512, 512, fb2, vwt, qvb, fb3);
-  gemm_tail<0, 1><<<dim3(4, 4), 256, 0, stream>>>(
-      fb3, owt, 512, 512, nullptr, nullptr, o_b, fb4);
-  gemm_tail<0, 1><<<dim3(4, 4), 256, 0, stream>>>(
-      fb4, f1t, 512, 512, nullptr, nullptr, ffn1_b, fb5);
-  ffn2_kernel<<<128, 256, 0, stream>>>(fb5, ffn2_w, ffn2_b, out);
-}
+    int r = (base == 0) ? 16 : 0;
+    k_gat1<<<8 * C, 256, 0, stream>>>(P, base);
+    k_att<<<C + r, 256, 0, stream>>>(P, base);
+    k_gat2<<<4 * C + r, 256, 0, stream>>>(P, base);
+  }
+  k_tail6<<<16, 256, 0, stream>>>(P);
+}
```
